# Kernel tuning notes

Hardware: AMD Instinct MI355X
Metric: run time of the kernel (lower is better)

The kernel has to match this reference:

```python
import jax, jax.numpy as jnp
import numpy as np

B, NAG = 8192, 16          # scenes, agents per scene
CIN, CH = 64, 128          # gnn_in_channels, gnn_out_channels
R2 = 8.0 * 8.0             # comm_range squared
BOX = 20.0                 # positions sampled uniformly in [0, BOX]^2


def _lin(k, fi, fo):
    k1, k2 = jax.random.split(k)
    s = 1.0 / np.sqrt(fi)
    W = jax.random.uniform(k1, (fi, fo), jnp.float32, -s, s)
    b = jax.random.uniform(k2, (fo,), jnp.float32, -s, s)
    return W, b


def setup_inputs() -> dict:
    key = jax.random.key(0)
    ks = jax.random.split(key, 10)
    x = jax.random.normal(ks[0], (B * NAG, CIN), jnp.float32)          # VAE mu per agent
    pos = jax.random.uniform(ks[1], (B, NAG, 2), jnp.float32) * BOX    # sensor xy positions
    W_rel1, b_rel1 = _lin(ks[2], CIN, CH)
    W_root1, _ = _lin(ks[3], CIN, CH)
    W_rel2, b_rel2 = _lin(ks[4], CH, CH)
    W_root2, _ = _lin(ks[5], CH, CH)
    Wh1, bh1 = _lin(ks[6], 2 * CH, 64)
    Wh2, bh2 = _lin(ks[7], 64, 32)
    Wh3, bh3 = _lin(ks[8], 32, 16)
    return dict(x=x, pos=pos, W_rel1=W_rel1, b_rel1=b_rel1, W_root1=W_root1,
                W_rel2=W_rel2, b_rel2=b_rel2, W_root2=W_root2,
                Wh1=Wh1, bh1=bh1, Wh2=Wh2, bh2=bh2, Wh3=Wh3, bh3=bh3)


def _graph_conv(h, adj, W_rel, b_rel, W_root):
    # PyG GraphConv (aggr='add'): out_i = W_rel @ sum_{j in N(i)} h_j + b_rel + W_root @ h_i
    nb = adj.shape[0]
    hb = h.reshape(nb, NAG, h.shape[-1])                 # [B, n, C]
    agg = jnp.einsum('bij,bjc->bic', adj, hb)            # neighbor sum within each scene
    return agg.reshape(h.shape[0], -1) @ W_rel + b_rel + h @ W_root


def reference(x, pos, W_rel1, b_rel1, W_root1, W_rel2, b_rel2, W_root2,
              Wh1, bh1, Wh2, bh2, Wh3, bh3):
    # radius_graph (batch-isolated, loop=False) as a per-scene dense mask
    diff = pos[:, :, None, :] - pos[:, None, :, :]       # [B, n, n, 2]
    d2 = jnp.sum(diff * diff, axis=-1)                   # [B, n, n]
    eye = jnp.eye(NAG, dtype=bool)
    adj = ((d2 <= R2) & ~eye).astype(x.dtype)            # [B, n, n]
    # Dropout(p=0.2) omitted (eval / deterministic reference).
    x1 = jax.nn.relu(_graph_conv(x, adj, W_rel1, b_rel1, W_root1))   # named 'x1' (inplace ReLU)
    x2 = jax.nn.relu(_graph_conv(x1, adj, W_rel2, b_rel2, W_root2))  # named 'x2' (inplace ReLU)
    h = jnp.concatenate([x1, x2], axis=-1)               # JumpingKnowledge('cat')
    h = jax.nn.relu(h @ Wh1 + bh1)
    h = jax.nn.relu(h @ Wh2 + bh2)
    out = h @ Wh3 + bh3                                  # [N, 16]
    return out.reshape(B, NAG, 16)
```

## Files before the change

### kernel.cpp

```cpp
#include <hip/hip_runtime.h>

#define NAG 16
#define SPB 4
#define NBLK 2048
#define TPB 512
#define R2f 64.0f

typedef unsigned short u16;
typedef __attribute__((ext_vector_type(8))) short short8;
typedef __attribute__((ext_vector_type(4))) float f32x4;

#define MFMA(a, b, c) __builtin_amdgcn_mfma_f32_16x16x32_bf16(a, b, c, 0, 0, 0)

#define OFF_B1 0
#define OFF_B2 16384
#define OFF_H1 49152
#define OFF_H2 65536
#define OFF_H3 67584
#define SWZ_UNITS 8512

__device__ __forceinline__ u16 f2b(float f) {
    unsigned u = __float_as_uint(f);
    unsigned r = u + 0x7FFFu + ((u >> 16) & 1u);
    return (u16)(r >> 16);
}
__device__ __forceinline__ unsigned rb(float f) {
    return (__float_as_uint(f) + 0x8000u) >> 16;
}
__device__ __forceinline__ unsigned pk2(float a, float b) {
    return ((__float_as_uint(a) + 0x8000u) >> 16) |
           ((__float_as_uint(b) + 0x8000u) & 0xFFFF0000u);
}

__global__ __launch_bounds__(256) void swizzle_w(
    const float* __restrict__ Wrel1, const float* __restrict__ Wroot1,
    const float* __restrict__ Wrel2, const float* __restrict__ Wroot2,
    const float* __restrict__ Wh1,  const float* __restrict__ Wh2,
    const float* __restrict__ Wh3,  u16* __restrict__ ws)
{
    const int u = blockIdx.x * 256 + threadIdx.x;
    if (u >= SWZ_UNITS) return;
    int v, T, N, ksplit;
    const float *W, *W2;
    u16* dst;
    if (u < 2048)      { v = u;        T = 8; N = 128; ksplit = 64;  W = Wroot1; W2 = Wrel1; dst = ws + OFF_B1 + v * 8; }
    else if (u < 6144) { v = u - 2048; T = 8; N = 128; ksplit = 128; W = Wroot2; W2 = Wrel2; dst = ws + OFF_B2 + v * 8; }
    else if (u < 8192) { v = u - 6144; T = 4; N = 64;  ksplit = 1 << 30; W = Wh1; W2 = Wh1; dst = ws + OFF_H1 + v * 8; }
    else if (u < 8448) { v = u - 8192; T = 2; N = 32;  ksplit = 1 << 30; W = Wh2; W2 = Wh2; dst = ws + OFF_H2 + v * 8; }
    else               { v = u - 8448; T = 1; N = 16;  ksplit = 1 << 30; W = Wh3; W2 = Wh3; dst = ws + OFF_H3 + v * 8; }
    const int lane = v & 63;
    const int t = (v >> 6) % T;
    const int s = (v >> 6) / T;
    const int n = t * 16 + (lane & 15);
    const int k0 = s * 32 + (lane >> 4) * 8;
    #pragma unroll
    for (int j = 0; j < 8; ++j) {
        const int k = k0 + j;
        const float val = (k < ksplit) ? W[k * N + n] : W2[(k - ksplit) * N + n];
        dst[j] = f2b(val);
    }
}

__device__ __forceinline__ short8 ldfrag(const u16* __restrict__ ws, int off,
                                         int T, int s, int tile, int lane) {
    return *(const short8*)(ws + off + (size_t)(((s * T + tile) * 64 + lane) * 8));
}

__device__ __forceinline__ short8 make_adjA(unsigned m, int q, int odd) {
    union { short8 v; unsigned u[4]; } r;
    const bool on = (q >> 1) == odd;
    const int base = (q & 1) * 8;
    #pragma unroll
    for (int jj = 0; jj < 4; ++jj) {
        const int k0 = base + 2 * jj;
        const unsigned lo = (on && ((m >> k0) & 1u)) ? 0x3F80u : 0u;
        const unsigned hi = (on && ((m >> (k0 + 1)) & 1u)) ? 0x3F80u : 0u;
        r.u[jj] = lo | (hi << 16);
    }
    return r.v;
}

__global__ __launch_bounds__(TPB) void gnn_fused6(
    const float* __restrict__ x, const float* __restrict__ pos,
    const float* __restrict__ brel1, const float* __restrict__ brel2,
    const float* __restrict__ bh1,  const float* __restrict__ bh2,
    const float* __restrict__ bh3,
    const u16* __restrict__ ws, float* __restrict__ out)
{
    __shared__ __align__(16) u16 pool[26624];
    __shared__ unsigned mask[64];
    u16* const xb  = pool;
    u16* const yT  = pool + 8704;
    u16* const x1b = pool + 17920;

    const int t = threadIdx.x;
    const int wv = t >> 6, lane = t & 63, ln = lane & 15, q = lane >> 4;
    const int c0 = 16 * wv;
    const size_t sA = (size_t)blockIdx.x * SPB;

    {
        const int r = t >> 3, co = (t & 7) * 8;
        const float* src = x + (sA * 16 + r) * 64 + co;
        const float4 v0 = *(const float4*)(src);
        const float4 v1 = *(const float4*)(src + 4);
        uint4 ua;
        ua.x = pk2(v0.x, v0.y); ua.y = pk2(v0.z, v0.w);
        ua.z = pk2(v1.x, v1.y); ua.w = pk2(v1.z, v1.w);
        *(uint4*)&xb[r * 136 + co] = ua;
    }
    if (t < 64) {
        const int g = t >> 4, a = t & 15;
        const float* pp = pos + (sA + g) * (NAG * 2);
        const float ax = pp[2 * a], ay = pp[2 * a + 1];
        unsigned m = 0;
        for (int j = 0; j < NAG; ++j) {
            const float dx = ax - pp[2 * j], dy = ay - pp[2 * j + 1];
            if (dx * dx + dy * dy <= R2f && j != a) m |= (1u << j);
        }
        mask[g * 16 + a] = m;
    }
    __syncthreads();

    short8 adjA[4];
    #pragma unroll
    for (int g = 0; g < 4; ++g) adjA[g] = make_adjA(mask[g * 16 + ln], q, g & 1);

    {
        short8 Brl[2], Bro[2], Af[4][2];
        #pragma unroll
        for (int s = 0; s < 2; ++s) {
            Brl[s] = ldfrag(ws, OFF_B1, 8, s + 2, wv, lane);
            Bro[s] = ldfrag(ws, OFF_B1, 8, s, wv, lane);
        }
        #pragma unroll
        for (int m = 0; m < 4; ++m) {
            Af[m][0] = *(const short8*)&xb[(m * 16 + ln) * 136 + q * 8];
            Af[m][1] = *(const short8*)&xb[(m * 16 + ln) * 136 + 32 + q * 8];
            f32x4 a0 = {0.f, 0.f, 0.f, 0.f};
            a0 = MFMA(Af[m][0], Brl[0], a0);
            a0 = MFMA(Af[m][1], Brl[1], a0);
            uint2 u0; u0.x = pk2(a0[0], a0[1]); u0.y = pk2(a0[2], a0[3]);
            *(uint2*)&yT[(c0 + ln) * 72 + m * 16 + q * 4] = u0;
        }
        short8 By[2];
        #pragma unroll
        for (int w = 0; w < 2; ++w)
            By[w] = *(const short8*)&yT[(c0 + ln) * 72 + w * 32 + q * 8];
        const float b0 = brel1[c0 + ln];
        #pragma unroll
        for (int g = 0; g < 4; ++g) {
            f32x4 a0 = {b0, b0, b0, b0};
            a0 = MFMA(Af[g][0], Bro[0], a0);
            a0 = MFMA(Af[g][1], Bro[1], a0);
            a0 = MFMA(adjA[g], By[g >> 1], a0);
            #pragma unroll
            for (int r = 0; r < 4; ++r)
                x1b[(g * 16 + q * 4 + r) * 136 + c0 + ln] = (u16)rb(fmaxf(a0[r], 0.f));
        }
    }
    __syncthreads();

    {
        short8 Brl[4];
        #pragma unroll
        for (int s = 0; s < 4; ++s) Brl[s] = ldfrag(ws, OFF_B2, 8, s + 4, wv, lane);
        #pragma unroll
        for (int m = 0; m < 4; ++m) {
            f32x4 a0 = {0.f, 0.f, 0.f, 0.f};
            #pragma unroll
            for (int s = 0; s < 4; ++s) {
                const short8 A = *(const short8*)&x1b[(m * 16 + ln) * 136 + s * 32 + q * 8];
                a0 = MFMA(A, Brl[s], a0);
            }
            uint2 u0; u0.x = pk2(a0[0], a0[1]); u0.y = pk2(a0[2], a0[3]);
            *(uint2*)&yT[(c0 + ln) * 72 + m * 16 + q * 4] = u0;
        }
        short8 By[2];
        #pragma unroll
        for (int w = 0; w < 2; ++w)
            By[w] = *(const short8*)&yT[(c0 + ln) * 72 + w * 32 + q * 8];
        short8 Bro[4];
        #pragma unroll
        for (int s = 0; s < 4; ++s) Bro[s] = ldfrag(ws, OFF_B2, 8, s, wv, lane);
        const float b0 = brel2[c0 + ln];
        #pragma unroll
        for (int g = 0; g < 4; ++g) {
            f32x4 a0 = {b0, b0, b0, b0};
            #pragma unroll
            for (int s = 0; s < 4; ++s) {
                const short8 A = *(const short8*)&x1b[(g * 16 + ln) * 136 + s * 32 + q * 8];
                a0 = MFMA(A, Bro[s], a0);
            }
            a0 = MFMA(adjA[g], By[g >> 1], a0);
            #pragma unroll
            for (int r = 0; r < 4; ++r)
                xb[(g * 16 + q * 4 + r) * 136 + c0 + ln] = (u16)rb(fmaxf(a0[r], 0.f));
        }
    }
    __syncthreads();

    {
        const int nt = wv & 3, mh = wv >> 2;
        short8 Bf[8];
        #pragma unroll
        for (int s = 0; s < 8; ++s) Bf[s] = ldfrag(ws, OFF_H1, 4, s, nt, lane);
        const float b = bh1[nt * 16 + ln];
        #pragma unroll
        for (int mi = 0; mi < 2; ++mi) {
            const int m = 2 * mh + mi;
            f32x4 a = {b, b, b, b}, c = {0.f, 0.f, 0.f, 0.f};
            #pragma unroll
            for (int s = 0; s < 4; ++s) {
                const short8 A1 = *(const short8*)&x1b[(m * 16 + ln) * 136 + s * 32 + q * 8];
                const short8 A2 = *(const short8*)&xb[(m * 16 + ln) * 136 + s * 32 + q * 8];
                a = MFMA(A1, Bf[s], a);
                c = MFMA(A2, Bf[s + 4], c);
            }
            #pragma unroll
            for (int r = 0; r < 4; ++r)
                yT[(m * 16 + q * 4 + r) * 72 + nt * 16 + ln] = (u16)rb(fmaxf(a[r] + c[r], 0.f));
        }
    }
    __syncthreads();

    if (wv < 4) {
        const u16* h1b = yT;
        u16* h2b = x1b;
        const short8 A0 = *(const short8*)&h1b[(wv * 16 + ln) * 72 + q * 8];
        const short8 A1 = *(const short8*)&h1b[(wv * 16 + ln) * 72 + 32 + q * 8];
        #pragma unroll
        for (int nt = 0; nt < 2; ++nt) {
            const short8 B0 = ldfrag(ws, OFF_H2, 2, 0, nt, lane);
            const short8 B1 = ldfrag(ws, OFF_H2, 2, 1, nt, lane);
            const float b = bh2[nt * 16 + ln];
            f32x4 a = {b, b, b, b};
            a = MFMA(A0, B0, a);
            a = MFMA(A1, B1, a);
            #pragma unroll
            for (int r = 0; r < 4; ++r)
                h2b[(wv * 16 + q * 4 + r) * 40 + nt * 16 + ln] = (u16)rb(fmaxf(a[r], 0.f));
        }
        const short8 A = *(const short8*)&h2b[(wv * 16 + ln) * 40 + q * 8];
        const short8 B = ldfrag(ws, OFF_H3, 1, 0, 0, lane);
        const float b = bh3[ln];
        f32x4 a = {b, b, b, b};
        a = MFMA(A, B, a);
        #pragma unroll
        for (int r = 0; r < 4; ++r)
            out[(sA * 16 + wv * 16 + q * 4 + r) * 16 + ln] = a[r];
    }
}

extern "C" void kernel_launch(void* const* d_in, const int* in_sizes, int n_in,
                              void* d_out, int out_size, void* d_ws, size_t ws_size,
                              hipStream_t stream) {
    const float* x      = (const float*)d_in[0];
    const float* pos    = (const float*)d_in[1];
    const float* Wrel1  = (const float*)d_in[2];
    const float* brel1  = (const float*)d_in[3];
    const float* Wroot1 = (const float*)d_in[4];
    const float* Wrel2  = (const float*)d_in[5];
    const float* brel2  = (const float*)d_in[6];
    const float* Wroot2 = (const float*)d_in[7];
    const float* Wh1    = (const float*)d_in[8];
    const float* bh1    = (const float*)d_in[9];
    const float* Wh2    = (const float*)d_in[10];
    const float* bh2    = (const float*)d_in[11];
    const float* Wh3    = (const float*)d_in[12];
    const float* bh3    = (const float*)d_in[13];
    u16* ws = (u16*)d_ws;

    swizzle_w<<<(SWZ_UNITS + 255) / 256, 256, 0, stream>>>(
        Wrel1, Wroot1, Wrel2, Wroot2, Wh1, Wh2, Wh3, ws);
    gnn_fused6<<<NBLK, TPB, 0, stream>>>(
        x, pos, brel1, brel2, bh1, bh2, bh3, ws, (float*)d_out);
}
```

Before: 126.6 us.

## Swap MFMA operand roles so outputs are stored as packed vector rows

Every MFMA is transposed so that weights become the A operand and activations the B operand. Each lane's four accumulator values then fall on consecutive channels, which allows packed 8-byte LDS stores, float4 bias loads and float4 global output writes in place of scalar 2-byte stores. The layer-1 and layer-2 loops are also regrouped into pairs of scenes, each pair sharing one yT read, to shorten live ranges. This trades some register-pressure and correctness risk in the transposed adjacency and weight fragment layouts for fewer LDS and global store instructions.

```diff
diff --git a/kernel.cpp b/kernel.cpp
--- a/kernel.cpp
+++ b/kernel.cpp
@@ -23,9 +23,6 @@
     unsigned u = __float_as_uint(f);
     unsigned r = u + 0x7FFFu + ((u >> 16) & 1u);
     return (u16)(r >> 16);
-}
-__device__ __forceinline__ unsigned rb(float f) {
-    return (__float_as_uint(f) + 0x8000u) >> 16;
 }
 __device__ __forceinline__ unsigned pk2(float a, float b) {
     return ((__float_as_uint(a) + 0x8000u) >> 16) |
@@ -66,7 +63,7 @@
     return *(const short8*)(ws + off + (size_t)(((s * T + tile) * 64 + lane) * 8));
 }
 
-__device__ __forceinline__ short8 make_adjA(unsigned m, int q, int odd) {
+__device__ __forceinline__ short8 make_adj(unsigned m, int q, int odd) {
     union { short8 v; unsigned u[4]; } r;
     const bool on = (q >> 1) == odd;
     const int base = (q & 1) * 8;
@@ -80,7 +77,14 @@
     return r.v;
 }
 
-__global__ __launch_bounds__(TPB) void gnn_fused6(
+__device__ __forceinline__ void relu_store4(u16* d, f32x4 a) {
+    uint2 u;
+    u.x = pk2(fmaxf(a[0], 0.f), fmaxf(a[1], 0.f));
+    u.y = pk2(fmaxf(a[2], 0.f), fmaxf(a[3], 0.f));
+    *(uint2*)d = u;
+}
+
+__global__ __launch_bounds__(TPB) void gnn_fused7(
     const float* __restrict__ x, const float* __restrict__ pos,
     const float* __restrict__ brel1, const float* __restrict__ brel2,
     const float* __restrict__ bh1,  const float* __restrict__ bh2,
@@ -121,133 +125,129 @@
     }
     __syncthreads();
 
-    short8 adjA[4];
+    short8 adjB[4];
     #pragma unroll
-    for (int g = 0; g < 4; ++g) adjA[g] = make_adjA(mask[g * 16 + ln], q, g & 1);
-
-    {
-        short8 Brl[2], Bro[2], Af[4][2];
+    for (int g = 0; g < 4; ++g) adjB[g] = make_adj(mask[g * 16 + ln], q, g & 1);
+
+    {
+        short8 Wrl[2], Wro[2];
         #pragma unroll
         for (int s = 0; s < 2; ++s) {
-            Brl[s] = ldfrag(ws, OFF_B1, 8, s + 2, wv, lane);
-            Bro[s] = ldfrag(ws, OFF_B1, 8, s, wv, lane);
-        }
-        #pragma unroll
-        for (int m = 0; m < 4; ++m) {
-            Af[m][0] = *(const short8*)&xb[(m * 16 + ln) * 136 + q * 8];
-            Af[m][1] = *(const short8*)&xb[(m * 16 + ln) * 136 + 32 + q * 8];
-            f32x4 a0 = {0.f, 0.f, 0.f, 0.f};
-            a0 = MFMA(Af[m][0], Brl[0], a0);
-            a0 = MFMA(Af[m][1], Brl[1], a0);
-            uint2 u0; u0.x = pk2(a0[0], a0[1]); u0.y = pk2(a0[2], a0[3]);
-            *(uint2*)&yT[(c0 + ln) * 72 + m * 16 + q * 4] = u0;
-        }
-        short8 By[2];
-        #pragma unroll
-        for (int w = 0; w < 2; ++w)
-            By[w] = *(const short8*)&yT[(c0 + ln) * 72 + w * 32 + q * 8];
-        const float b0 = brel1[c0 + ln];
-        #pragma unroll
-        for (int g = 0; g < 4; ++g) {
-            f32x4 a0 = {b0, b0, b0, b0};
-            a0 = MFMA(Af[g][0], Bro[0], a0);
-            a0 = MFMA(Af[g][1], Bro[1], a0);
-            a0 = MFMA(adjA[g], By[g >> 1], a0);
-            #pragma unroll
-            for (int r = 0; r < 4; ++r)
-                x1b[(g * 16 + q * 4 + r) * 136 + c0 + ln] = (u16)rb(fmaxf(a0[r], 0.f));
-        }
-    }
-    __syncthreads();
-
-    {
-        short8 Brl[4];
-        #pragma unroll
-        for (int s = 0; s < 4; ++s) Brl[s] = ldfrag(ws, OFF_B2, 8, s + 4, wv, lane);
-        #pragma unroll
-        for (int m = 0; m < 4; ++m) {
-            f32x4 a0 = {0.f, 0.f, 0.f, 0.f};
+            Wrl[s] = ldfrag(ws, OFF_B1, 8, s + 2, wv, lane);
+            Wro[s] = ldfrag(ws, OFF_B1, 8, s, wv, lane);
+        }
+        const float4 bv = *(const float4*)(brel1 + c0 + q * 4);
+        #pragma unroll
+        for (int p = 0; p < 2; ++p) {
+            short8 Bx[2][2];
+            #pragma unroll
+            for (int gi = 0; gi < 2; ++gi) {
+                const int g = 2 * p + gi;
+                Bx[gi][0] = *(const short8*)&xb[(g * 16 + ln) * 136 + q * 8];
+                Bx[gi][1] = *(const short8*)&xb[(g * 16 + ln) * 136 + 32 + q * 8];
+                f32x4 ay = {0.f, 0.f, 0.f, 0.f};
+                ay = MFMA(Bx[gi][0], Wrl[0], ay);
+                ay = MFMA(Bx[gi][1], Wrl[1], ay);
+                uint2 u; u.x = pk2(ay[0], ay[1]); u.y = pk2(ay[2], ay[3]);
+                *(uint2*)&yT[(c0 + ln) * 72 + g * 16 + q * 4] = u;
+            }
+            const short8 yA = *(const short8*)&yT[(c0 + ln) * 72 + p * 32 + q * 8];
+            #pragma unroll
+            for (int gi = 0; gi < 2; ++gi) {
+                const int g = 2 * p + gi;
+                f32x4 a = {bv.x, bv.y, bv.z, bv.w};
+                a = MFMA(Wro[0], Bx[gi][0], a);
+                a = MFMA(Wro[1], Bx[gi][1], a);
+                a = MFMA(yA, adjB[g], a);
+                relu_store4(&x1b[(g * 16 + ln) * 136 + c0 + q * 4], a);
+            }
+        }
+    }
+    __syncthreads();
+
+    {
+        short8 Wrl[4], Wro[4];
+        #pragma unroll
+        for (int s = 0; s < 4; ++s) {
+            Wrl[s] = ldfrag(ws, OFF_B2, 8, s + 4, wv, lane);
+            Wro[s] = ldfrag(ws, OFF_B2, 8, s, wv, lane);
+        }
+        const float4 bv = *(const float4*)(brel2 + c0 + q * 4);
+        #pragma unroll
+        for (int p = 0; p < 2; ++p) {
+            short8 Bx[2][4];
+            #pragma unroll
+            for (int gi = 0; gi < 2; ++gi) {
+                const int g = 2 * p + gi;
+                f32x4 ay = {0.f, 0.f, 0.f, 0.f};
+                #pragma unroll
+                for (int s = 0; s < 4; ++s) {
+                    Bx[gi][s] = *(const short8*)&x1b[(g * 16 + ln) * 136 + s * 32 + q * 8];
+                    ay = MFMA(Bx[gi][s], Wrl[s], ay);
+                }
+                uint2 u; u.x = pk2(ay[0], ay[1]); u.y = pk2(ay[2], ay[3]);
+                *(uint2*)&yT[(c0 + ln) * 72 + g * 16 + q * 4] = u;
+            }
+            const short8 yA = *(const short8*)&yT[(c0 + ln) * 72 + p * 32 + q * 8];
+            #pragma unroll
+            for (int gi = 0; gi < 2; ++gi) {
+                const int g = 2 * p + gi;
+                f32x4 a = {bv.x, bv.y, bv.z, bv.w};
+                #pragma unroll
+                for (int s = 0; s < 4; ++s) a = MFMA(Wro[s], Bx[gi][s], a);
+                a = MFMA(yA, adjB[g], a);
+                relu_store4(&xb[(g * 16 + ln) * 136 + c0 + q * 4], a);
+            }
+        }
+    }
+    __syncthreads();
+
+    {
+        const int mt = wv & 3, h = wv >> 2;
+        short8 Wf[8];
+        #pragma unroll
+        for (int s = 0; s < 8; ++s) Wf[s] = ldfrag(ws, OFF_H1, 4, s, mt, lane);
+        const float4 bv = *(const float4*)(bh1 + mt * 16 + q * 4);
+        u16* const h1 = yT;
+        #pragma unroll
+        for (int ni = 0; ni < 2; ++ni) {
+            const int nt = 2 * h + ni;
+            f32x4 a = {bv.x, bv.y, bv.z, bv.w};
             #pragma unroll
             for (int s = 0; s < 4; ++s) {
-                const short8 A = *(const short8*)&x1b[(m * 16 + ln) * 136 + s * 32 + q * 8];
-                a0 = MFMA(A, Brl[s], a0);
-            }
-            uint2 u0; u0.x = pk2(a0[0], a0[1]); u0.y = pk2(a0[2], a0[3]);
-            *(uint2*)&yT[(c0 + ln) * 72 + m * 16 + q * 4] = u0;
-        }
-        short8 By[2];
-        #pragma unroll
-        for (int w = 0; w < 2; ++w)
-            By[w] = *(const short8*)&yT[(c0 + ln) * 72 + w * 32 + q * 8];
-        short8 Bro[4];
-        #pragma unroll
-        for (int s = 0; s < 4; ++s) Bro[s] = ldfrag(ws, OFF_B2, 8, s, wv, lane);
-        const float b0 = brel2[c0 + ln];
-        #pragma unroll
-        for (int g = 0; g < 4; ++g) {
-            f32x4 a0 = {b0, b0, b0, b0};
-            #pragma unroll
-            for (int s = 0; s < 4; ++s) {
-                const short8 A = *(const short8*)&x1b[(g * 16 + ln) * 136 + s * 32 + q * 8];
-                a0 = MFMA(A, Bro[s], a0);
-            }
-            a0 = MFMA(adjA[g], By[g >> 1], a0);
-            #pragma unroll
-            for (int r = 0; r < 4; ++r)
-                xb[(g * 16 + q * 4 + r) * 136 + c0 + ln] = (u16)rb(fmaxf(a0[r], 0.f));
-        }
-    }
-    __syncthreads();
-
-    {
-        const int nt = wv & 3, mh = wv >> 2;
-        short8 Bf[8];
-        #pragma unroll
-        for (int s = 0; s < 8; ++s) Bf[s] = ldfrag(ws, OFF_H1, 4, s, nt, lane);
-        const float b = bh1[nt * 16 + ln];
-        #pragma unroll
-        for (int mi = 0; mi < 2; ++mi) {
-            const int m = 2 * mh + mi;
-            f32x4 a = {b, b, b, b}, c = {0.f, 0.f, 0.f, 0.f};
-            #pragma unroll
-            for (int s = 0; s < 4; ++s) {
-                const short8 A1 = *(const short8*)&x1b[(m * 16 + ln) * 136 + s * 32 + q * 8];
-                const short8 A2 = *(const short8*)&xb[(m * 16 + ln) * 136 + s * 32 + q * 8];
-                a = MFMA(A1, Bf[s], a);
-                c = MFMA(A2, Bf[s + 4], c);
-            }
-            #pragma unroll
-            for (int r = 0; r < 4; ++r)
-                yT[(m * 16 + q * 4 + r) * 72 + nt * 16 + ln] = (u16)rb(fmaxf(a[r] + c[r], 0.f));
+                const short8 B1 = *(const short8*)&x1b[(nt * 16 + ln) * 136 + s * 32 + q * 8];
+                const short8 B2 = *(const short8*)&xb[(nt * 16 + ln) * 136 + s * 32 + q * 8];
+                a = MFMA(Wf[s], B1, a);
+                a = MFMA(Wf[s + 4], B2, a);
+            }
+            relu_store4(&h1[(nt * 16 + ln) * 72 + mt * 16 + q * 4], a);
         }
     }
     __syncthreads();
 
     if (wv < 4) {
-        const u16* h1b = yT;
-        u16* h2b = x1b;
-        const short8 A0 = *(const short8*)&h1b[(wv * 16 + ln) * 72 + q * 8];
-        const short8 A1 = *(const short8*)&h1b[(wv * 16 + ln) * 72 + 32 + q * 8];
-        #pragma unroll
-        for (int nt = 0; nt < 2; ++nt) {
-            const short8 B0 = ldfrag(ws, OFF_H2, 2, 0, nt, lane);
-            const short8 B1 = ldfrag(ws, OFF_H2, 2, 1, nt, lane);
-            const float b = bh2[nt * 16 + ln];
-            f32x4 a = {b, b, b, b};
-            a = MFMA(A0, B0, a);
-            a = MFMA(A1, B1, a);
-            #pragma unroll
-            for (int r = 0; r < 4; ++r)
-                h2b[(wv * 16 + q * 4 + r) * 40 + nt * 16 + ln] = (u16)rb(fmaxf(a[r], 0.f));
-        }
-        const short8 A = *(const short8*)&h2b[(wv * 16 + ln) * 40 + q * 8];
-        const short8 B = ldfrag(ws, OFF_H3, 1, 0, 0, lane);
-        const float b = bh3[ln];
-        f32x4 a = {b, b, b, b};
-        a = MFMA(A, B, a);
-        #pragma unroll
-        for (int r = 0; r < 4; ++r)
-            out[(sA * 16 + wv * 16 + q * 4 + r) * 16 + ln] = a[r];
+        const int sc = wv;
+        const u16* const h1 = yT;
+        u16* const h2 = x1b;
+        const short8 Bh0 = *(const short8*)&h1[(sc * 16 + ln) * 72 + q * 8];
+        const short8 Bh1f = *(const short8*)&h1[(sc * 16 + ln) * 72 + 32 + q * 8];
+        #pragma unroll
+        for (int mt = 0; mt < 2; ++mt) {
+            const short8 W0 = ldfrag(ws, OFF_H2, 2, 0, mt, lane);
+            const short8 W1 = ldfrag(ws, OFF_H2, 2, 1, mt, lane);
+            const float4 bv = *(const float4*)(bh2 + mt * 16 + q * 4);
+            f32x4 a = {bv.x, bv.y, bv.z, bv.w};
+            a = MFMA(W0, Bh0, a);
+            a = MFMA(W1, Bh1f, a);
+            relu_store4(&h2[(sc * 16 + ln) * 40 + mt * 16 + q * 4], a);
+        }
+        const short8 Bh2 = *(const short8*)&h2[(sc * 16 + ln) * 40 + q * 8];
+        const short8 W3 = ldfrag(ws, OFF_H3, 1, 0, 0, lane);
+        const float4 bv = *(const float4*)(bh3 + q * 4);
+        f32x4 a = {bv.x, bv.y, bv.z, bv.w};
+        a = MFMA(W3, Bh2, a);
+        float4 o; o.x = a[0]; o.y = a[1]; o.z = a[2]; o.w = a[3];
+        *(float4*)(out + ((sA + sc) * 16 + ln) * 16 + q * 4) = o;
     }
 }
 
@@ -272,6 +272,6 @@
 
     swizzle_w<<<(SWZ_UNITS + 255) / 256, 256, 0, stream>>>(
         Wrel1, Wroot1, Wrel2, Wroot2, Wh1, Wh2, Wh3, ws);
-    gnn_fused6<<<NBLK, TPB, 0, stream>>>(
+    gnn_fused7<<<NBLK, TPB, 0, stream>>>(
         x, pos, brel1, brel2, bh1, bh2, bh3, ws, (float*)d_out);
 }
```

Measured after the change: 127.6 us. No clear change (+0.8%).
